# Kernel optimization log

Measured on AMD Instinct MI355X. Metric: run time of the kernel, lower is better.

## Reference

```python
import jax, jax.numpy as jnp
import numpy as np

NEG_SLOPE = 0.2
BN_EPS = 1e-5


def gat_conv(x, src, dst, W, att_src, att_dst, bias):
    """PyG-style GATConv (eval mode, shared src/dst lin, self-loops already in src/dst)."""
    N = x.shape[0]
    H, C = att_src.shape
    h = (x @ W).reshape(N, H, C)                      # [N,H,C]
    a_s = jnp.sum(h * att_src[None], axis=-1)         # [N,H]
    a_d = jnp.sum(h * att_dst[None], axis=-1)         # [N,H]
    e = jax.nn.leaky_relu(a_s[src] + a_d[dst], NEG_SLOPE)   # [E,H]
    # segment softmax over edges grouped by destination node
    m = jax.ops.segment_max(e, dst, num_segments=N)   # [N,H]
    ee = jnp.exp(e - m[dst])
    denom = jax.ops.segment_sum(ee, dst, num_segments=N)
    alpha = ee / (denom[dst] + 1e-16)                 # [E,H]
    msg = h[src] * alpha[..., None]                   # [E,H,C]
    out = jax.ops.segment_sum(msg, dst, num_segments=N)  # [N,H,C]
    return out.reshape(N, H * C) + bias


def setup_inputs() -> dict:
    key = jax.random.key(0)
    ks = jax.random.split(key, 12)
    N, E, Fin, C1, H, Fout = 50000, 800000, 128, 16, 8, 40
    HC = H * C1
    x = jax.random.normal(ks[0], (N, Fin), jnp.float32)
    edge_index = jax.random.randint(ks[1], (2, E), 0, N, dtype=jnp.int32)
    W1 = jax.random.normal(ks[2], (Fin, HC), jnp.float32) / np.sqrt(Fin).astype(np.float32)
    att_src1 = jax.random.normal(ks[3], (H, C1), jnp.float32) * 0.1
    att_dst1 = jax.random.normal(ks[4], (H, C1), jnp.float32) * 0.1
    b1 = jnp.zeros((HC,), jnp.float32)
    bn_gamma = jnp.ones((HC,), jnp.float32)
    bn_beta = jnp.zeros((HC,), jnp.float32)
    bn_mean = jnp.zeros((HC,), jnp.float32)
    bn_var = jnp.ones((HC,), jnp.float32)
    W2 = jax.random.normal(ks[5], (HC, Fout), jnp.float32) / np.sqrt(HC).astype(np.float32)
    att_src2 = jax.random.normal(ks[6], (1, Fout), jnp.float32) * 0.1
    att_dst2 = jax.random.normal(ks[7], (1, Fout), jnp.float32) * 0.1
    b2 = jnp.zeros((Fout,), jnp.float32)
    return {"x": x, "edge_index": edge_index, "W1": W1, "att_src1": att_src1,
            "att_dst1": att_dst1, "b1": b1, "bn_gamma": bn_gamma, "bn_beta": bn_beta,
            "bn_mean": bn_mean, "bn_var": bn_var, "W2": W2, "att_src2": att_src2,
            "att_dst2": att_dst2, "b2": b2}


def reference(x, edge_index, W1, att_src1, att_dst1, b1, bn_gamma, bn_beta,
              bn_mean, bn_var, W2, att_src2, att_dst2, b2):
    N = x.shape[0]
    loop = jnp.arange(N, dtype=edge_index.dtype)
    src = jnp.concatenate([edge_index[0], loop])   # PyG add_self_loops=True
    dst = jnp.concatenate([edge_index[1], loop])
    h = gat_conv(x, src, dst, W1, att_src1, att_dst1, b1)
    h = (h - bn_mean) * jax.lax.rsqrt(bn_var + BN_EPS) * bn_gamma + bn_beta  # BN eval
    h = jax.nn.elu(h)
    out = gat_conv(h, src, dst, W2, att_src2, att_dst2, b2)
    return jax.nn.log_softmax(out, axis=1)
```

## Files before the change

### kernel.cpp

```cpp
#include <hip/hip_runtime.h>
#include <hip/hip_bf16.h>
#include <math.h>

#define LRELU(v) ((v) > 0.f ? (v) : 0.2f * (v))

typedef __attribute__((ext_vector_type(8))) short bf16x8;
typedef __attribute__((ext_vector_type(4))) float f32x4;

__device__ inline unsigned int f2bf(float f) {
  unsigned int u = __float_as_uint(f);
  return (u + 0x7fffu + ((u >> 16) & 1u)) >> 16;
}

__global__ __launch_bounds__(256) void wtrans_k(const float* __restrict__ W,
                                                unsigned short* __restrict__ wt)
{
  int idx = blockIdx.x * 256 + threadIdx.x;
  int k = idx >> 7, c = idx & 127;
  wt[c * 128 + k] = (unsigned short)f2bf(W[idx]);
}

#define LDA 152
__global__ __launch_bounds__(256) void gemm1_k(
    const float* __restrict__ x, const unsigned short* __restrict__ wt,
    const float* __restrict__ atts, const float* __restrict__ attd,
    unsigned short* __restrict__ h1s, float* __restrict__ as1,
    float* __restrict__ ad1, int N)
{
  __shared__ unsigned short xs[64 * LDA];
  const int t = threadIdx.x;
  const int row0 = blockIdx.x * 64;
  const int lane = t & 63, w = t >> 6;

#pragma unroll
  for (int i = 0; i < 8; ++i) {
    int idx = t + i * 256;
    int r = idx >> 5, kq = idx & 31;
    int rr = row0 + r;
    float4 v = make_float4(0.f, 0.f, 0.f, 0.f);
    if (rr < N) v = *reinterpret_cast<const float4*>(&x[(size_t)rr * 128 + kq * 4]);
    unsigned int p0 = f2bf(v.x) | (f2bf(v.y) << 16);
    unsigned int p1 = f2bf(v.z) | (f2bf(v.w) << 16);
    *reinterpret_cast<uint2*>(&xs[r * LDA + kq * 4]) = make_uint2(p0, p1);
  }
  __syncthreads();

  const int l16 = lane & 15, lhi = lane >> 4;
  const int nb0 = w * 32;
  f32x4 acc[4][2];
#pragma unroll
  for (int m = 0; m < 4; ++m)
#pragma unroll
    for (int n = 0; n < 2; ++n) acc[m][n] = (f32x4){0.f, 0.f, 0.f, 0.f};

#pragma unroll
  for (int ks = 0; ks < 4; ++ks) {
    bf16x8 bf[2];
#pragma unroll
    for (int n = 0; n < 2; ++n) {
      int col = nb0 + n * 16 + l16;
      bf[n] = *reinterpret_cast<const bf16x8*>(&wt[col * 128 + ks * 32 + 8 * lhi]);
    }
#pragma unroll
    for (int m = 0; m < 4; ++m) {
      bf16x8 af = *reinterpret_cast<const bf16x8*>(
          &xs[(m * 16 + l16) * LDA + ks * 32 + 8 * lhi]);
      acc[m][0] = __builtin_amdgcn_mfma_f32_16x16x32_bf16(af, bf[0], acc[m][0], 0, 0, 0);
      acc[m][1] = __builtin_amdgcn_mfma_f32_16x16x32_bf16(af, bf[1], acc[m][1], 0, 0, 0);
    }
  }

#pragma unroll
  for (int n = 0; n < 2; ++n) {
    int col = nb0 + n * 16 + l16;
    float av = atts[col], dv = attd[col];
    int head = w * 2 + n;
#pragma unroll
    for (int m = 0; m < 4; ++m) {
#pragma unroll
      for (int r = 0; r < 4; ++r) {
        int row = row0 + m * 16 + lhi * 4 + r;
        float v = acc[m][n][r];
        float s = v * av, d = v * dv;
        s += __shfl_xor(s, 1); s += __shfl_xor(s, 2);
        s += __shfl_xor(s, 4); s += __shfl_xor(s, 8);
        d += __shfl_xor(d, 1); d += __shfl_xor(d, 2);
        d += __shfl_xor(d, 4); d += __shfl_xor(d, 8);
        if (row < N) {
          h1s[(size_t)row * 128 + col] = (unsigned short)f2bf(v);
          if (l16 == 0) { as1[row * 8 + head] = s; ad1[row * 8 + head] = d; }
        }
      }
    }
  }
}

#define NBUK_MAX 256

__global__ __launch_bounds__(256) void bhist_k(const int* __restrict__ ei,
                                               int E, int N,
                                               int* __restrict__ bcnt, int nbuk)
{
  __shared__ int h[NBUK_MAX];
  for (int i = threadIdx.x; i < nbuk; i += 256) h[i] = 0;
  __syncthreads();
  const int Etot = E + N;
  const int base = blockIdx.x * 4096;
#pragma unroll 4
  for (int i = threadIdx.x; i < 4096; i += 256) {
    int e = base + i;
    if (e < Etot) {
      int d = (e < E) ? ei[E + e] : (e - E);
      atomicAdd(&h[d >> 8], 1);
    }
  }
  __syncthreads();
  for (int i = threadIdx.x; i < nbuk; i += 256)
    if (h[i]) atomicAdd(&bcnt[i], h[i]);
}

__global__ __launch_bounds__(256) void bscan_k(const int* __restrict__ bcnt,
                                               int* __restrict__ bbase,
                                               int* __restrict__ bpos, int nbuk)
{
  __shared__ int wsum[4];
  const int t = threadIdx.x, lane = t & 63, w = t >> 6;
  int v = (t < nbuk) ? bcnt[t] : 0;
  int incl = v;
#pragma unroll
  for (int off = 1; off < 64; off <<= 1) {
    int y = __shfl_up(incl, off);
    if (lane >= off) incl += y;
  }
  if (lane == 63) wsum[w] = incl;
  __syncthreads();
  if (t == 0) {
    int a = wsum[0], b = wsum[1], c = wsum[2];
    wsum[3] = a + b + c + wsum[3];
    wsum[1] = a; wsum[2] = a + b; wsum[0] = 0;
  }
  __syncthreads();
  if (t == 0) wsum[3] = wsum[2];
  __syncthreads();
  __shared__ int wtot[4];
  if (lane == 63) wtot[w] = incl;
  __syncthreads();
  if (t == 0) {
    int a = wtot[0], b = wtot[1], c = wtot[2];
    wsum[0] = 0; wsum[1] = a; wsum[2] = a + b; wsum[3] = a + b + c;
  }
  __syncthreads();
  int ex = wsum[w] + incl - v;
  if (t < nbuk) { bbase[t] = ex; bpos[t] = ex; }
  if (t == nbuk - 1) bbase[nbuk] = ex + v;
}

__global__ __launch_bounds__(256) void bscat_k(const int* __restrict__ ei,
                                               int E, int N,
                                               int* __restrict__ bpos,
                                               unsigned int* __restrict__ stg,
                                               int nbuk)
{
  __shared__ int h[NBUK_MAX], gp[NBUK_MAX], cur[NBUK_MAX];
  for (int i = threadIdx.x; i < nbuk; i += 256) { h[i] = 0; cur[i] = 0; }
  __syncthreads();
  const int Etot = E + N;
  const int base = blockIdx.x * 4096;
  int s[16], d[16];
#pragma unroll
  for (int i = 0; i < 16; ++i) {
    int e = base + i * 256 + threadIdx.x;
    if (e < Etot) {
      if (e < E) { s[i] = ei[e]; d[i] = ei[E + e]; }
      else       { s[i] = d[i] = e - E; }
      atomicAdd(&h[d[i] >> 8], 1);
    } else d[i] = -1;
  }
  __syncthreads();
  for (int i = threadIdx.x; i < nbuk; i += 256)
    gp[i] = h[i] ? atomicAdd(&bpos[i], h[i]) : 0;
  __syncthreads();
#pragma unroll
  for (int i = 0; i < 16; ++i) {
    if (d[i] >= 0) {
      int b = d[i] >> 8;
      int r = atomicAdd(&cur[b], 1);
      stg[gp[b] + r] = ((unsigned int)s[i] << 8) | (unsigned int)(d[i] & 255);
    }
  }
}

#define CCAP 4992
__global__ __launch_bounds__(512) void csr_k(const unsigned int* __restrict__ stg,
                                             const int* __restrict__ bbase,
                                             int* __restrict__ rowptr,
                                             int* __restrict__ col,
                                             int N, int nbuk)
{
  __shared__ int nh[256], nb[257], cur[256], wsum[4];
  __shared__ int cstage[CCAP];
  const int b = blockIdx.x, t = threadIdx.x;
  const int n0 = b << 8;
  const int e0 = bbase[b], e1 = bbase[b + 1], cnt = e1 - e0;
  if (t < 256) { nh[t] = 0; cur[t] = 0; }
  __syncthreads();
  for (int i = t; i < cnt; i += 512)
    atomicAdd(&nh[stg[e0 + i] & 255u], 1);
  __syncthreads();
  if (t < 256) {
    const int lane = t & 63, w = t >> 6;
    int v = nh[t], incl = v;
#pragma unroll
    for (int off = 1; off < 64; off <<= 1) {
      int y = __shfl_up(incl, off);
      if (lane >= off) incl += y;
    }
    if (lane == 63) wsum[w] = incl;
    __syncthreads();
    if (t == 0) {
      int a = wsum[0], bb = wsum[1], c = wsum[2];
      wsum[0] = 0; wsum[1] = a; wsum[2] = a + bb; wsum[3] = a + bb + c;
    }
    __syncthreads();
    int ex = wsum[w] + incl - v;
    nb[t] = ex;
    if (t == 255) nb[256] = ex + v;
  } else {
    __syncthreads();
    __syncthreads();
  }
  __syncthreads();
  const int nnodes = min(256, N - n0);
  for (int i = t; i < nnodes; i += 512) rowptr[n0 + i] = e0 + nb[i];
  if (b == nbuk - 1 && t == 0) rowptr[N] = e1;
  for (int i = t; i < cnt; i += 512) {
    unsigned int sd = stg[e0 + i];
    int li = sd & 255u;
    int p = nb[li] + atomicAdd(&cur[li], 1);
    int sv = (int)(sd >> 8);
    if (p < CCAP) cstage[p] = sv; else col[e0 + p] = sv;
  }
  __syncthreads();
  const int lim = min(cnt, CCAP);
  for (int i = t; i < lim; i += 512) col[e0 + i] = cstage[i];
}

__global__ __launch_bounds__(256) void agg1_k(
    const unsigned int* __restrict__ h1b, const float* __restrict__ as1,
    const float* __restrict__ ad1, const int* __restrict__ rowptr,
    const int* __restrict__ col, const float* __restrict__ b1,
    const float* __restrict__ gamma, const float* __restrict__ beta,
    const float* __restrict__ mean, const float* __restrict__ var,
    float* __restrict__ hmid, int N)
{
  const int wid = threadIdx.x >> 6, lane = threadIdx.x & 63;
  const int n = blockIdx.x * 4 + wid;
  if (n >= N) return;
  const int h = lane >> 3;
  const int c0 = lane * 2;
  const float adv = ad1[n * 8 + h];
  float den = 0.f, a0 = 0.f, a1 = 0.f;
  const int jb = rowptr[n], je = rowptr[n + 1];
  int j = jb;
  for (; j + 8 <= je; j += 8) {
    int s[8];
#pragma unroll
    for (int q = 0; q < 8; ++q) s[q] = col[j + q];
    float e[8];
#pragma unroll
    for (int q = 0; q < 8; ++q) e[q] = as1[s[q] * 8 + h];
    unsigned int u[8];
#pragma unroll
    for (int q = 0; q < 8; ++q) u[q] = h1b[(size_t)s[q] * 64 + lane];
#pragma unroll
    for (int q = 0; q < 8; ++q) {
      float p = __expf(LRELU(e[q] + adv));
      den += p;
      a0 += p * __uint_as_float(u[q] << 16);
      a1 += p * __uint_as_float(u[q] & 0xffff0000u);
    }
  }
  for (; j < je; ++j) {
    int s = col[j];
    float e = LRELU(as1[s * 8 + h] + adv);
    unsigned int u = h1b[(size_t)s * 64 + lane];
    float p = __expf(e);
    den += p;
    a0 += p * __uint_as_float(u << 16);
    a1 += p * __uint_as_float(u & 0xffff0000u);
  }
  float r = 1.f / (den + 1e-16f);
  float o0 = a0 * r + b1[c0];
  float o1 = a1 * r + b1[c0 + 1];
  float bn0 = (o0 - mean[c0]) * rsqrtf(var[c0] + 1e-5f) * gamma[c0] + beta[c0];
  float bn1 = (o1 - mean[c0 + 1]) * rsqrtf(var[c0 + 1] + 1e-5f) * gamma[c0 + 1] + beta[c0 + 1];
  float2 o;
  o.x = bn0 > 0.f ? bn0 : expm1f(bn0);
  o.y = bn1 > 0.f ? bn1 : expm1f(bn1);
  *reinterpret_cast<float2*>(&hmid[(size_t)n * 128 + c0]) = o;
}

__global__ __launch_bounds__(256) void gemm2_k(
    const float* __restrict__ hmid, const float* __restrict__ W2,
    const float* __restrict__ atts, const float* __restrict__ attd,
    float* __restrict__ h2p, float* __restrict__ as2, float* __restrict__ ad2,
    int N)
{
  __shared__ float hm[128 * 36];
  __shared__ float w2t[40 * 36];
  const int t = threadIdx.x;
  const int n0 = blockIdx.x * 128;
  const int lane = t & 63, w = t >> 6;
  const int ng = lane >> 3, cg = lane & 7;
  const int nloc = w * 32 + ng * 4;

  float acc[4][5];
#pragma unroll
  for (int i = 0; i < 4; ++i)
#pragma unroll
    for (int j = 0; j < 5; ++j) acc[i][j] = 0.f;

  for (int kc = 0; kc < 4; ++kc) {
    __syncthreads();
#pragma unroll
    for (int i = 0; i < 4; ++i) {
      int idx = t + i * 256;
      int r = idx >> 3, kq = idx & 7;
      int rr = n0 + r;
      float4 v = make_float4(0.f, 0.f, 0.f, 0.f);
      if (rr < N)
        v = *reinterpret_cast<const float4*>(&hmid[(size_t)rr * 128 + kc * 32 + kq * 4]);
      *reinterpret_cast<float4*>(&hm[r * 36 + kq * 4]) = v;
    }
#pragma unroll
    for (int i = 0; i < 5; ++i) {
      int flat = t + i * 256;
      int c = flat >> 5, kk = flat & 31;
      w2t[c * 36 + kk] = W2[(size_t)(kc * 32 + kk) * 40 + c];
    }
    __syncthreads();
#pragma unroll
    for (int k4 = 0; k4 < 8; ++k4) {
      float hv[4][4];
#pragma unroll
      for (int i = 0; i < 4; ++i)
        *reinterpret_cast<float4*>(hv[i]) =
            *reinterpret_cast<const float4*>(&hm[(nloc + i) * 36 + k4 * 4]);
      float wv[5][4];
#pragma unroll
      for (int j = 0; j < 5; ++j)
        *reinterpret_cast<float4*>(wv[j]) =
            *reinterpret_cast<const float4*>(&w2t[(cg * 5 + j) * 36 + k4 * 4]);
#pragma unroll
      for (int i = 0; i < 4; ++i)
#pragma unroll
        for (int j = 0; j < 5; ++j)
#pragma unroll
          for (int kk = 0; kk < 4; ++kk)
            acc[i][j] += hv[i][kk] * wv[j][kk];
    }
  }

  float asv[5], adv[5];
#pragma unroll
  for (int j = 0; j < 5; ++j) { asv[j] = atts[cg * 5 + j]; adv[j] = attd[cg * 5 + j]; }
#pragma unroll
  for (int i = 0; i < 4; ++i) {
    int n = n0 + nloc + i;
    if (n >= N) continue;
    float ps = 0.f, pd = 0.f;
#pragma unroll
    for (int j = 0; j < 5; ++j) { ps += acc[i][j] * asv[j]; pd += acc[i][j] * adv[j]; }
#pragma unroll
    for (int off = 1; off < 8; off <<= 1) {
      ps += __shfl_xor(ps, off);
      pd += __shfl_xor(pd, off);
    }
#pragma unroll
    for (int j = 0; j < 5; ++j) h2p[(size_t)n * 40 + cg * 5 + j] = acc[i][j];
    if (cg == 0) { as2[n] = ps; ad2[n] = pd; }
  }
}

__global__ __launch_bounds__(256) void agg2_k(
    const float* __restrict__ h2p, const float* __restrict__ as2,
    const float* __restrict__ ad2, const int* __restrict__ rowptr,
    const int* __restrict__ col, const float* __restrict__ b2,
    float* __restrict__ out, int N)
{
  const int wid = threadIdx.x >> 6, lane = threadIdx.x & 63;
  const int n = blockIdx.x * 4 + wid;
  if (n >= N) return;
  const bool act = lane < 40;
  const int cl = act ? lane : 39;
  const float adv = ad2[n];
  float den = 0.f, acc = 0.f;
  const int jb = rowptr[n], je = rowptr[n + 1];
  int j = jb;
  for (; j + 4 <= je; j += 4) {
    int s0 = col[j], s1 = col[j + 1], s2 = col[j + 2], s3 = col[j + 3];
    float e0 = as2[s0], e1 = as2[s1], e2 = as2[s2], e3 = as2[s3];
    float v0 = h2p[(size_t)s0 * 40 + cl];
    float v1 = h2p[(size_t)s1 * 40 + cl];
    float v2 = h2p[(size_t)s2 * 40 + cl];
    float v3 = h2p[(size_t)s3 * 40 + cl];
    e0 = LRELU(e0 + adv); e1 = LRELU(e1 + adv);
    e2 = LRELU(e2 + adv); e3 = LRELU(e3 + adv);
    float p0 = __expf(e0), p1 = __expf(e1);
    float p2 = __expf(e2), p3 = __expf(e3);
    den += p0; den += p1; den += p2; den += p3;
    acc += p0 * v0; acc += p1 * v1; acc += p2 * v2; acc += p3 * v3;
  }
  for (; j < je; ++j) {
    int s = col[j];
    float e = LRELU(as2[s] + adv);
    float v = h2p[(size_t)s * 40 + cl];
    float p = __expf(e);
    den += p;
    acc += p * v;
  }
  float o = acc / (den + 1e-16f) + b2[cl];
  float mv = act ? o : -INFINITY;
#pragma unroll
  for (int off = 1; off < 64; off <<= 1) mv = fmaxf(mv, __shfl_xor(mv, off));
  float ex = act ? __expf(o - mv) : 0.f;
#pragma unroll
  for (int off = 1; off < 64; off <<= 1) ex += __shfl_xor(ex, off);
  float ls = logf(ex);
  if (act) out[(size_t)n * 40 + lane] = o - mv - ls;
}

extern "C" void kernel_launch(void* const* d_in, const int* in_sizes, int n_in,
                              void* d_out, int out_size, void* d_ws,
                              size_t ws_size, hipStream_t stream)
{
  const float* x      = (const float*)d_in[0];
  const int*   ei     = (const int*)d_in[1];
  const float* W1     = (const float*)d_in[2];
  const float* att_s1 = (const float*)d_in[3];
  const float* att_d1 = (const float*)d_in[4];
  const float* b1     = (const float*)d_in[5];
  const float* gamma  = (const float*)d_in[6];
  const float* beta   = (const float*)d_in[7];
  const float* mean   = (const float*)d_in[8];
  const float* var    = (const float*)d_in[9];
  const float* W2     = (const float*)d_in[10];
  const float* att_s2 = (const float*)d_in[11];
  const float* att_d2 = (const float*)d_in[12];
  const float* b2     = (const float*)d_in[13];
  float* out = (float*)d_out;

  const int N = in_sizes[0] / 128;
  const int E = in_sizes[1] / 2;
  const int Etot = E + N;
  const int nbuk = (N + 255) >> 8;
  const int nchunk = (Etot + 4095) / 4096;

  char* ws = (char*)d_ws;
  size_t off = 0;
  auto alloc = [&](size_t bytes) -> void* {
    void* p = ws + off;
    off = (off + bytes + 255) & ~(size_t)255;
    return p;
  };
  unsigned short* h1s = (unsigned short*)alloc((size_t)N * 128 * 2);
  float* as1  = (float*)alloc((size_t)N * 8 * 4);
  float* ad1  = (float*)alloc((size_t)N * 8 * 4);
  float* hmid = (float*)alloc((size_t)N * 128 * 4);
  int* rowptr = (int*)alloc((size_t)(N + 1) * 4);
  int* col    = (int*)alloc((size_t)Etot * 4);
  unsigned int* stg = (unsigned int*)alloc((size_t)Etot * 4);
  int* bcnt   = (int*)alloc(NBUK_MAX * 4);
  int* bbase  = (int*)alloc((NBUK_MAX + 1) * 4);
  int* bpos   = (int*)alloc(NBUK_MAX * 4);
  unsigned short* wt = (unsigned short*)alloc(16384 * 2);
  float* h2p = (float*)h1s;
  float* as2 = as1;
  float* ad2 = ad1;

  hipMemsetAsync(bcnt, 0, NBUK_MAX * 4, stream);

  wtrans_k<<<64, 256, 0, stream>>>(W1, wt);
  gemm1_k<<<(N + 63) / 64, 256, 0, stream>>>(x, wt, att_s1, att_d1,
                                             h1s, as1, ad1, N);
  bhist_k<<<nchunk, 256, 0, stream>>>(ei, E, N, bcnt, nbuk);
  bscan_k<<<1, 256, 0, stream>>>(bcnt, bbase, bpos, nbuk);
  bscat_k<<<nchunk, 256, 0, stream>>>(ei, E, N, bpos, stg, nbuk);
  csr_k<<<nbuk, 512, 0, stream>>>(stg, bbase, rowptr, col, N, nbuk);

  agg1_k<<<(N + 3) / 4, 256, 0, stream>>>((const unsigned int*)h1s, as1, ad1,
                                          rowptr, col, b1,
                                          gamma, beta, mean, var, hmid, N);
  gemm2_k<<<(N + 127) / 128, 256, 0, stream>>>(hmid, W2, att_s2, att_d2,
                                               h2p, as2, ad2, N);
  agg2_k<<<(N + 3) / 4, 256, 0, stream>>>(h2p, as2, ad2, rowptr, col, b2,
                                          out, N);
}
```

Measured before the change: 177.6 us.

## Split edges across lane groups with vector loads in both aggregation kernels

agg1 now has four 16-lane groups per wavefront, each handling a different edge and reading 16 bytes (8 bf16 channels) per lane, with partial sums combined by cross-lane shuffles. agg2 likewise uses three 20-lane groups that read float2 pairs and process up to 6 edges per iteration instead of a serial 4-edge unroll. The aim is more independent gathers in flight and fewer load instructions per edge on the memory-bound aggregation, at the cost of shuffle reductions and idle lanes on tail iterations. Dead redundant scan code in bscan is also removed.

```diff
diff --git a/kernel.cpp b/kernel.cpp
--- a/kernel.cpp
+++ b/kernel.cpp
@@ -123,7 +123,7 @@
                                                int* __restrict__ bbase,
                                                int* __restrict__ bpos, int nbuk)
 {
-  __shared__ int wsum[4];
+  __shared__ int wsum[4], wtot[4];
   const int t = threadIdx.x, lane = t & 63, w = t >> 6;
   int v = (t < nbuk) ? bcnt[t] : 0;
   int incl = v;
@@ -132,17 +132,6 @@
     int y = __shfl_up(incl, off);
     if (lane >= off) incl += y;
   }
-  if (lane == 63) wsum[w] = incl;
-  __syncthreads();
-  if (t == 0) {
-    int a = wsum[0], b = wsum[1], c = wsum[2];
-    wsum[3] = a + b + c + wsum[3];
-    wsum[1] = a; wsum[2] = a + b; wsum[0] = 0;
-  }
-  __syncthreads();
-  if (t == 0) wsum[3] = wsum[2];
-  __syncthreads();
-  __shared__ int wtot[4];
   if (lane == 63) wtot[w] = incl;
   __syncthreads();
   if (t == 0) {
@@ -256,48 +245,59 @@
   const int wid = threadIdx.x >> 6, lane = threadIdx.x & 63;
   const int n = blockIdx.x * 4 + wid;
   if (n >= N) return;
-  const int h = lane >> 3;
-  const int c0 = lane * 2;
+  const int el = lane >> 4;
+  const int cl = lane & 15;
+  const int h  = cl >> 1;
   const float adv = ad1[n * 8 + h];
-  float den = 0.f, a0 = 0.f, a1 = 0.f;
+  float den = 0.f;
+  float acc[8];
+#pragma unroll
+  for (int k = 0; k < 8; ++k) acc[k] = 0.f;
   const int jb = rowptr[n], je = rowptr[n + 1];
-  int j = jb;
-  for (; j + 8 <= je; j += 8) {
-    int s[8];
-#pragma unroll
-    for (int q = 0; q < 8; ++q) s[q] = col[j + q];
-    float e[8];
-#pragma unroll
-    for (int q = 0; q < 8; ++q) e[q] = as1[s[q] * 8 + h];
-    unsigned int u[8];
-#pragma unroll
-    for (int q = 0; q < 8; ++q) u[q] = h1b[(size_t)s[q] * 64 + lane];
-#pragma unroll
-    for (int q = 0; q < 8; ++q) {
-      float p = __expf(LRELU(e[q] + adv));
-      den += p;
-      a0 += p * __uint_as_float(u[q] << 16);
-      a1 += p * __uint_as_float(u[q] & 0xffff0000u);
-    }
-  }
-  for (; j < je; ++j) {
-    int s = col[j];
-    float e = LRELU(as1[s * 8 + h] + adv);
-    unsigned int u = h1b[(size_t)s * 64 + lane];
-    float p = __expf(e);
-    den += p;
-    a0 += p * __uint_as_float(u << 16);
-    a1 += p * __uint_as_float(u & 0xffff0000u);
-  }
-  float r = 1.f / (den + 1e-16f);
-  float o0 = a0 * r + b1[c0];
-  float o1 = a1 * r + b1[c0 + 1];
-  float bn0 = (o0 - mean[c0]) * rsqrtf(var[c0] + 1e-5f) * gamma[c0] + beta[c0];
-  float bn1 = (o1 - mean[c0 + 1]) * rsqrtf(var[c0 + 1] + 1e-5f) * gamma[c0 + 1] + beta[c0 + 1];
-  float2 o;
-  o.x = bn0 > 0.f ? bn0 : expm1f(bn0);
-  o.y = bn1 > 0.f ? bn1 : expm1f(bn1);
-  *reinterpret_cast<float2*>(&hmid[(size_t)n * 128 + c0]) = o;
+  for (int j = jb; j < je; j += 8) {
+    int j0 = j + el, j1 = j + 4 + el;
+    bool v0 = j0 < je, v1 = j1 < je;
+    int s0 = col[v0 ? j0 : je - 1];
+    int s1 = col[v1 ? j1 : je - 1];
+    float e0 = as1[s0 * 8 + h];
+    float e1 = as1[s1 * 8 + h];
+    uint4 u0 = *reinterpret_cast<const uint4*>(&h1b[(size_t)s0 * 64 + cl * 4]);
+    uint4 u1 = *reinterpret_cast<const uint4*>(&h1b[(size_t)s1 * 64 + cl * 4]);
+    float p0 = v0 ? __expf(LRELU(e0 + adv)) : 0.f;
+    float p1 = v1 ? __expf(LRELU(e1 + adv)) : 0.f;
+    den += p0 + p1;
+    unsigned int w0[4] = {u0.x, u0.y, u0.z, u0.w};
+    unsigned int w1[4] = {u1.x, u1.y, u1.z, u1.w};
+#pragma unroll
+    for (int k = 0; k < 4; ++k) {
+      acc[2 * k]     += p0 * __uint_as_float(w0[k] << 16);
+      acc[2 * k + 1] += p0 * __uint_as_float(w0[k] & 0xffff0000u);
+      acc[2 * k]     += p1 * __uint_as_float(w1[k] << 16);
+      acc[2 * k + 1] += p1 * __uint_as_float(w1[k] & 0xffff0000u);
+    }
+  }
+  den += __shfl_xor(den, 16); den += __shfl_xor(den, 32);
+#pragma unroll
+  for (int k = 0; k < 8; ++k) {
+    acc[k] += __shfl_xor(acc[k], 16);
+    acc[k] += __shfl_xor(acc[k], 32);
+  }
+  if (el == 0) {
+    float r = 1.f / (den + 1e-16f);
+    int c0 = cl * 8;
+    float o[8];
+#pragma unroll
+    for (int k = 0; k < 8; ++k) {
+      int c = c0 + k;
+      float ov = acc[k] * r + b1[c];
+      float bn = (ov - mean[c]) * rsqrtf(var[c] + 1e-5f) * gamma[c] + beta[c];
+      o[k] = bn > 0.f ? bn : expm1f(bn);
+    }
+    *reinterpret_cast<float4*>(&hmid[(size_t)n * 128 + c0]) =
+        make_float4(o[0], o[1], o[2], o[3]);
+    *reinterpret_cast<float4*>(&hmid[(size_t)n * 128 + c0 + 4]) =
+        make_float4(o[4], o[5], o[6], o[7]);
+  }
 }
 
 __global__ __launch_bounds__(256) void gemm2_k(
@@ -391,43 +391,46 @@
   const int wid = threadIdx.x >> 6, lane = threadIdx.x & 63;
   const int n = blockIdx.x * 4 + wid;
   if (n >= N) return;
-  const bool act = lane < 40;
-  const int cl = act ? lane : 39;
+  const int el = (lane >= 40) ? 2 : (lane >= 20 ? 1 : 0);
+  const int cl = lane - el * 20;
+  const int c0 = (cl < 20 ? cl : 19) * 2;
+  const bool lv = lane < 60;
   const float adv = ad2[n];
-  float den = 0.f, acc = 0.f;
+  float den = 0.f, a0 = 0.f, a1 = 0.f;
   const int jb = rowptr[n], je = rowptr[n + 1];
-  int j = jb;
-  for (; j + 4 <= je; j += 4) {
-    int s0 = col[j], s1 = col[j + 1], s2 = col[j + 2], s3 = col[j + 3];
-    float e0 = as2[s0], e1 = as2[s1], e2 = as2[s2], e3 = as2[s3];
-    float v0 = h2p[(size_t)s0 * 40 + cl];
-    float v1 = h2p[(size_t)s1 * 40 + cl];
-    float v2 = h2p[(size_t)s2 * 40 + cl];
-    float v3 = h2p[(size_t)s3 * 40 + cl];
-    e0 = LRELU(e0 + adv); e1 = LRELU(e1 + adv);
-    e2 = LRELU(e2 + adv); e3 = LRELU(e3 + adv);
-    float p0 = __expf(e0), p1 = __expf(e1);
-    float p2 = __expf(e2), p3 = __expf(e3);
-    den += p0; den += p1; den += p2; den += p3;
-    acc += p0 * v0; acc += p1 * v1; acc += p2 * v2; acc += p3 * v3;
-  }
-  for (; j < je; ++j) {
-    int s = col[j];
-    float e = LRELU(as2[s] + adv);
-    float v = h2p[(size_t)s * 40 + cl];
-    float p = __expf(e);
-    den += p;
-    acc += p * v;
-  }
-  float o = acc / (den + 1e-16f) + b2[cl];
-  float mv = act ? o : -INFINITY;
-#pragma unroll
-  for (int off = 1; off < 64; off <<= 1) mv = fmaxf(mv, __shfl_xor(mv, off));
-  float ex = act ? __expf(o - mv) : 0.f;
-#pragma unroll
-  for (int off = 1; off < 64; off <<= 1) ex += __shfl_xor(ex, off);
+  for (int j = jb; j < je; j += 6) {
+    int j0 = j + el, j1 = j + 3 + el;
+    bool v0 = lv && (j0 < je), v1 = lv && (j1 < je);
+    int s0 = col[v0 ? j0 : je - 1];
+    int s1 = col[v1 ? j1 : je - 1];
+    float e0 = as2[s0], e1 = as2[s1];
+    float2 f0 = *reinterpret_cast<const float2*>(&h2p[(size_t)s0 * 40 + c0]);
+    float2 f1 = *reinterpret_cast<const float2*>(&h2p[(size_t)s1 * 40 + c0]);
+    float p0 = v0 ? __expf(LRELU(e0 + adv)) : 0.f;
+    float p1 = v1 ? __expf(LRELU(e1 + adv)) : 0.f;
+    den += p0 + p1;
+    a0 += p0 * f0.x + p1 * f1.x;
+    a1 += p0 * f0.y + p1 * f1.y;
+  }
+  float dt = __shfl(den, 0) + __shfl(den, 20) + __shfl(den, 40);
+  int base = (lane < 20) ? lane : 0;
+  float a0t = __shfl(a0, base) + __shfl(a0, base + 20) + __shfl(a0, base + 40);
+  float a1t = __shfl(a1, base) + __shfl(a1, base + 20) + __shfl(a1, base + 40);
+  const bool act = lane < 20;
+  float r = 1.f / (dt + 1e-16f);
+  float o0 = a0t * r + b2[c0];
+  float o1 = a1t * r + b2[c0 + 1];
+  float mv = act ? fmaxf(o0, o1) : -INFINITY;
+#pragma unroll
+  for (int off = 1; off < 32; off <<= 1) mv = fmaxf(mv, __shfl_xor(mv, off));
+  float ex = act ? (__expf(o0 - mv) + __expf(o1 - mv)) : 0.f;
+#pragma unroll
+  for (int off = 1; off < 32; off <<= 1) ex += __shfl_xor(ex, off);
   float ls = logf(ex);
-  if (act) out[(size_t)n * 40 + lane] = o - mv - ls;
+  if (act) {
+    float2 ov = make_float2(o0 - mv - ls, o1 - mv - ls);
+    *reinterpret_cast<float2*>(&out[(size_t)n * 40 + c0]) = ov;
+  }
 }
 
 extern "C" void kernel_launch(void* const* d_in, const int* in_sizes, int n_in,
```

Result: slower. 211.2 us (+18.9%).
